# Optimization experiments

Hardware: AMD Instinct MI355X
Metric: run time of the kernel (lower is better)

## Reference

```python
import jax, jax.numpy as jnp
import numpy as np

NUM_GRIDS = 8

def _rbf(x):
    # FastKAN-style radial basis over a fixed grid on [-2, 2]
    grid = jnp.linspace(-2.0, 2.0, NUM_GRIDS).astype(x.dtype)
    h = 4.0 / (NUM_GRIDS - 1)  # grid spacing used as RBF bandwidth
    z = (x[..., None] - grid) / h
    return jnp.exp(-z * z)  # (..., D, G)

def _spline_layer(x, base_w, base_b, spline_w, spline_b):
    # base path: Linear(silu(x)); spline path: Linear(rbf features)
    base = jax.nn.silu(x) @ base_w.T + base_b
    feats = _rbf(x).reshape(x.shape[:-1] + (x.shape[-1] * NUM_GRIDS,))
    return base + feats @ spline_w.T + spline_b


def setup_inputs() -> dict:
    key = jax.random.key(0)
    ks = jax.random.split(key, 12)
    B, Sx, Sy, D = 4, 1024, 1024, 256
    H1, H2 = 128, 64
    def lin(k, o, i):
        return (jax.random.normal(k, (o, i), jnp.float32) / np.sqrt(i)).astype(jnp.float32)
    return {
        "x": jax.random.normal(ks[0], (B, Sx, D), jnp.float32),
        "y": jax.random.normal(ks[1], (B, Sy, D), jnp.float32),
        "base_w1x": lin(ks[2], H1, D), "base_b1x": jnp.zeros((H1,), jnp.float32),
        "spline_w1x": lin(ks[3], H1, D * NUM_GRIDS), "spline_b1x": jnp.zeros((H1,), jnp.float32),
        "base_w2x": lin(ks[4], H2, H1), "base_b2x": jnp.zeros((H2,), jnp.float32),
        "spline_w2x": lin(ks[5], H2, H1 * NUM_GRIDS), "spline_b2x": jnp.zeros((H2,), jnp.float32),
        "base_w1y": lin(ks[6], H1, D), "base_b1y": jnp.zeros((H1,), jnp.float32),
        "spline_w1y": lin(ks[7], H1, D * NUM_GRIDS), "spline_b1y": jnp.zeros((H1,), jnp.float32),
        "base_w2y": lin(ks[8], H2, H1), "base_b2y": jnp.zeros((H2,), jnp.float32),
        "spline_w2y": lin(ks[9], H2, H1 * NUM_GRIDS), "spline_b2y": jnp.zeros((H2,), jnp.float32),
        "final_w": lin(ks[10], 1, 2 * H2), "final_b": jnp.zeros((1,), jnp.float32),
    }


def reference(x, y,
              base_w1x, base_b1x, spline_w1x, spline_b1x,
              base_w2x, base_b2x, spline_w2x, spline_b2x,
              base_w1y, base_b1y, spline_w1y, spline_b1y,
              base_w2y, base_b2y, spline_w2y, spline_b2y,
              final_w, final_b):
    # Per-branch spline stacks: (B, S, D) -> (B, S, H2)
    hx = _spline_layer(_spline_layer(x, base_w1x, base_b1x, spline_w1x, spline_b1x),
                       base_w2x, base_b2x, spline_w2x, spline_b2x)
    hy = _spline_layer(_spline_layer(y, base_w1y, base_b1y, spline_w1y, spline_b1y),
                       base_w2y, base_b2y, spline_w2y, spline_b2y)
    # The original expands to (B, Sx, Sy, 2*H2), applies the affine final
    # layer, then means over all Sx*Sy pairs. By linearity this equals two
    # independent seq-means projected by the split weight, avoiding the
    # quadratic intermediate while computing identical math.
    H2 = hx.shape[-1]
    wx, wy = final_w[:, :H2], final_w[:, H2:]
    out = hx.mean(axis=1) @ wx.T + hy.mean(axis=1) @ wy.T + final_b  # (B, 1)
    return out
```

## Files before the change

kernel.cpp:

```cpp
#include <hip/hip_runtime.h>

typedef __attribute__((ext_vector_type(8))) short short8;
typedef __attribute__((ext_vector_type(16))) float floatx16;


__device__ __forceinline__ unsigned short f2bf(float f) {
  union { float f; unsigned u; } v; v.f = f;
  unsigned r = v.u + 0x7fffu + ((v.u >> 16) & 1u);
  return (unsigned short)(r >> 16);
}

__global__ __launch_bounds__(512) void prep_frags(
    const float* __restrict__ bw1x, const float* __restrict__ sw1x,
    const float* __restrict__ bb1x, const float* __restrict__ sb1x,
    const float* __restrict__ bw2x, const float* __restrict__ sw2x,
    const float* __restrict__ bb2x, const float* __restrict__ sb2x,
    const float* __restrict__ bw1y, const float* __restrict__ sw1y,
    const float* __restrict__ bb1y, const float* __restrict__ sb1y,
    const float* __restrict__ bw2y, const float* __restrict__ sw2y,
    const float* __restrict__ bb2y, const float* __restrict__ sb2y,
    uint4* __restrict__ B1fx, uint4* __restrict__ B1fy,
    uint4* __restrict__ B2fx, uint4* __restrict__ B2fy,
    float* __restrict__ b1x, float* __restrict__ b1y,
    float* __restrict__ b2x, float* __restrict__ b2y,
    int* __restrict__ cnt)
{
  int idx = blockIdx.x * 512 + threadIdx.x;
  if (idx < 2 * 36864) {
    int sid = idx / 36864;
    int rem = idx - sid * 36864;
    int q = rem >> 6, l = rem & 63;
    int nc = q & 3, t9 = q >> 2;
    int j = t9 % 9, ds = t9 / 9;
    const float* bw = sid ? bw1y : bw1x;
    const float* sw = sid ? sw1y : sw1x;
    uint4* dst = sid ? B1fy : B1fx;
    int o = nc * 32 + (l & 31);
    int dbase = ds * 16 + (l >> 5) * 8;
    unsigned short eh[8];
    #pragma unroll
    for (int i = 0; i < 8; ++i) {
      int d = dbase + i;
      float wv = (j == 0) ? bw[o * 256 + d] : sw[o * 2048 + d * 8 + (j - 1)];
      eh[i] = f2bf(wv);
    }
    uint4 oh;
    oh.x = (unsigned)eh[0] | ((unsigned)eh[1] << 16);
    oh.y = (unsigned)eh[2] | ((unsigned)eh[3] << 16);
    oh.z = (unsigned)eh[4] | ((unsigned)eh[5] << 16);
    oh.w = (unsigned)eh[6] | ((unsigned)eh[7] << 16);
    dst[q * 64 + l] = oh;
  } else if (idx < 2 * 36864 + 2 * 9216) {
    int i2 = idx - 2 * 36864;
    int sid = i2 / 9216;
    int rem = i2 - sid * 9216;
    int q2 = rem >> 6, l = rem & 63;
    int nc = q2 & 1, t9 = q2 >> 1;
    int j = t9 % 9, w = t9 / 9;
    const float* bw = sid ? bw2y : bw2x;
    const float* sw = sid ? sw2y : sw2x;
    uint4* dst = sid ? B2fy : B2fx;
    int o = nc * 32 + (l & 31);
    int dbase = w * 16 + (l >> 5) * 8;
    unsigned short eh[8];
    #pragma unroll
    for (int i = 0; i < 8; ++i) {
      int d = dbase + i;
      float wv = (j == 0) ? bw[o * 128 + d] : sw[o * 1024 + d * 8 + (j - 1)];
      eh[i] = f2bf(wv);
    }
    uint4 oh;
    oh.x = (unsigned)eh[0] | ((unsigned)eh[1] << 16);
    oh.y = (unsigned)eh[2] | ((unsigned)eh[3] << 16);
    oh.z = (unsigned)eh[4] | ((unsigned)eh[5] << 16);
    oh.w = (unsigned)eh[6] | ((unsigned)eh[7] << 16);
    dst[q2 * 64 + l] = oh;
  } else {
    int i2 = idx - (2 * 36864 + 2 * 9216);
    if (i2 < 128)      b1x[i2]       = bb1x[i2]       + sb1x[i2];
    else if (i2 < 256) b1y[i2 - 128] = bb1y[i2 - 128] + sb1y[i2 - 128];
    else if (i2 < 320) b2x[i2 - 256] = bb2x[i2 - 256] + sb2x[i2 - 256];
    else if (i2 < 384) b2y[i2 - 320] = bb2y[i2 - 320] + sb2y[i2 - 320];
    else if (i2 < 388) cnt[i2 - 384] = 0;
  }
}

__global__ __launch_bounds__(512, 2) void fused_kernel(
    const float* __restrict__ Xx, const float* __restrict__ Xy,
    const uint4* __restrict__ B1fx, const uint4* __restrict__ B1fy,
    const uint4* __restrict__ B2fx, const uint4* __restrict__ B2fy,
    const float* __restrict__ b1x_, const float* __restrict__ b1y_,
    const float* __restrict__ b2x_, const float* __restrict__ b2y_,
    const float* __restrict__ finw, const float* __restrict__ finb,
    float* __restrict__ partial, int* __restrict__ cnt,
    float* __restrict__ out)
{
  __shared__ __align__(16) char smem[51232];
  float* xsh  = (float*)smem;
  float* S0   = (float*)smem;
  float* S1   = (float*)(smem + 16384);
  float* h1s  = (float*)(smem + 33792);
  float* redw = (float*)(smem + 51200);

  const int t    = threadIdx.x;
  const int bid  = blockIdx.x;
  const int sid  = bid >> 7;
  const int m    = bid & 127;
  const int wave = t >> 6;
  const int l    = t & 63;
  const int lc   = l & 31;
  const int lk   = l >> 5;

  const float* X  = sid ? Xy : Xx;
  const uint4* B1 = sid ? B1fy : B1fx;
  const uint4* B2 = sid ? B2fy : B2fx;
  const float* b1 = sid ? b1y_ : b1x_;
  const float* b2 = sid ? b2y_ : b2x_;

  {
    int row = t >> 4, col = (t & 15) * 16;
    const float* src = X + (size_t)(m * 32 + row) * 256 + col;
    #pragma unroll
    for (int q = 0; q < 4; ++q)
      *(float4*)(xsh + row * 264 + col + q * 4) = *(const float4*)(src + q * 4);
  }
  __syncthreads();

  float xr0[8], xr1[8];
  {
    int cb = wave * 32 + lk * 8;
    float4 v0 = *(const float4*)(xsh + lc * 264 + cb);
    float4 v1 = *(const float4*)(xsh + lc * 264 + cb + 4);
    float4 u0 = *(const float4*)(xsh + lc * 264 + cb + 16);
    float4 u1 = *(const float4*)(xsh + lc * 264 + cb + 20);
    xr0[0]=v0.x; xr0[1]=v0.y; xr0[2]=v0.z; xr0[3]=v0.w;
    xr0[4]=v1.x; xr0[5]=v1.y; xr0[6]=v1.z; xr0[7]=v1.w;
    xr1[0]=u0.x; xr1[1]=u0.y; xr1[2]=u0.z; xr1[3]=u0.w;
    xr1[4]=u1.x; xr1[5]=u1.y; xr1[6]=u1.z; xr1[7]=u1.w;
  }
  __syncthreads();

  floatx16 acc[4] = {};

  auto loadB1 = [&](int s, uint4* bf) {
    int j = s >> 1, ds = wave * 2 + (s & 1);
    const uint4* bp = B1 + (size_t)((ds * 9 + j) * 4) * 64 + l;
    #pragma unroll
    for (int nc = 0; nc < 4; ++nc) bf[nc] = bp[nc * 64];
  };
  auto computeB1 = [&](int s, const uint4* bf) {
    int j = s >> 1;
    const float* xr = (s & 1) ? xr1 : xr0;
    float f[8];
    if (j == 0) {
      #pragma unroll
      for (int i = 0; i < 8; ++i)
        f[i] = __fdividef(xr[i], 1.f + __expf(-xr[i]));
    } else {
      float g = -2.f + (float)(j - 1) * (4.f / 7.f);
      #pragma unroll
      for (int i = 0; i < 8; ++i) {
        float z = (xr[i] - g) * 1.75f;
        f[i] = __expf(-z * z);
      }
    }
    short8 a;
    #pragma unroll
    for (int i = 0; i < 8; ++i) a[i] = (short)f2bf(f[i]);
    #pragma unroll
    for (int nc = 0; nc < 4; ++nc) {
      short8 bh = __builtin_bit_cast(short8, bf[nc]);
      acc[nc] = __builtin_amdgcn_mfma_f32_32x32x16_bf16(a, bh, acc[nc], 0, 0, 0);
    }
  };

  {
    uint4 bfE[4], bfO[4];
    loadB1(0, bfE);
    #pragma unroll 1
    for (int s = 0; s < 18; s += 2) {
      loadB1(s + 1, bfO);
      computeB1(s, bfE);
      if (s + 2 < 18) loadB1(s + 2, bfE);
      computeB1(s + 1, bfO);
    }
  }

  auto st = [&](float* Sb) {
    #pragma unroll
    for (int nc = 0; nc < 4; ++nc)
      #pragma unroll
      for (int r = 0; r < 16; ++r) {
        int row = (r & 3) + 8 * (r >> 2) + 4 * lk;
        Sb[row * 128 + nc * 32 + lc] = acc[nc][r];
      }
  };
  auto ad = [&](const float* Sb) {
    #pragma unroll
    for (int nc = 0; nc < 4; ++nc)
      #pragma unroll
      for (int r = 0; r < 16; ++r) {
        int row = (r & 3) + 8 * (r >> 2) + 4 * lk;
        acc[nc][r] += Sb[row * 128 + nc * 32 + lc];
      }
  };
  __syncthreads();
  if (wave == 1) st(S0);
  if (wave == 3) st(S1);
  __syncthreads();
  if (wave == 0) ad(S0);
  if (wave == 2) ad(S1);
  __syncthreads();
  if (wave == 5) st(S0);
  if (wave == 7) st(S1);
  __syncthreads();
  if (wave == 4) ad(S0);
  if (wave == 6) ad(S1);
  __syncthreads();
  if (wave == 2) st(S0);
  if (wave == 6) st(S1);
  __syncthreads();
  if (wave == 0) ad(S0);
  if (wave == 4) ad(S1);
  __syncthreads();
  if (wave == 4) st(S0);
  __syncthreads();
  if (wave == 0) {
    ad(S0);
    #pragma unroll
    for (int nc = 0; nc < 4; ++nc)
      #pragma unroll
      for (int r = 0; r < 16; ++r) {
        int row = (r & 3) + 8 * (r >> 2) + 4 * lk;
        int col = nc * 32 + lc;
        h1s[row * 136 + col] = acc[nc][r] + b1[col];
      }
  }
  __syncthreads();

  floatx16 acc2[2] = {};

  auto loadB2 = [&](int s, uint4* cf) {
    const uint4* bp = B2 + (size_t)((wave * 9 + s) * 2) * 64 + l;
    #pragma unroll
    for (int nc = 0; nc < 2; ++nc) cf[nc] = bp[nc * 64];
  };

  uint4 cfE[2], cfO[2];
  loadB2(0, cfE);

  float hr[8];
  {
    int cb = wave * 16 + lk * 8;
    float4 v0 = *(const float4*)(h1s + lc * 136 + cb);
    float4 v1 = *(const float4*)(h1s + lc * 136 + cb + 4);
    hr[0]=v0.x; hr[1]=v0.y; hr[2]=v0.z; hr[3]=v0.w;
    hr[4]=v1.x; hr[5]=v1.y; hr[6]=v1.z; hr[7]=v1.w;
  }

  auto computeB2 = [&](int s, const uint4* cf) {
    float f[8];
    if (s == 0) {
      #pragma unroll
      for (int i = 0; i < 8; ++i)
        f[i] = __fdividef(hr[i], 1.f + __expf(-hr[i]));
    } else {
      float g = -2.f + (float)(s - 1) * (4.f / 7.f);
      #pragma unroll
      for (int i = 0; i < 8; ++i) {
        float z = (hr[i] - g) * 1.75f;
        f[i] = __expf(-z * z);
      }
    }
    short8 a;
    #pragma unroll
    for (int i = 0; i < 8; ++i) a[i] = (short)f2bf(f[i]);
    #pragma unroll
    for (int nc = 0; nc < 2; ++nc) {
      short8 bh = __builtin_bit_cast(short8, cf[nc]);
      acc2[nc] = __builtin_amdgcn_mfma_f32_32x32x16_bf16(a, bh, acc2[nc], 0, 0, 0);
    }
  };

  #pragma unroll 1
  for (int s = 0; s < 8; s += 2) {
    loadB2(s + 1, cfO);
    computeB2(s, cfE);
    loadB2(s + 2, cfE);
    computeB2(s + 1, cfO);
  }
  computeB2(8, cfE);

  const float* wf = finw + sid * 64;
  {
    float w0 = wf[lc], w1v = wf[32 + lc];
    float pz = 0.f;
    #pragma unroll
    for (int r = 0; r < 16; ++r) pz += acc2[0][r] * w0 + acc2[1][r] * w1v;
    #pragma unroll
    for (int off = 32; off > 0; off >>= 1) pz += __shfl_down(pz, off, 64);
    if (l == 0) redw[wave] = pz;
  }
  __syncthreads();

  if (wave == 0) {
    const int b    = m >> 5;
    const int slot = sid * 32 + (m & 31);
    float v = (l < 8) ? redw[l] : 0.f;
    v += 32.f * b2[l] * wf[l];
    #pragma unroll
    for (int off = 32; off > 0; off >>= 1) v += __shfl_down(v, off, 64);
    int old = 0;
    if (l == 0) {
      partial[b * 64 + slot] = v;
      __threadfence();
      old = atomicAdd(&cnt[b], 1);
    }
    int bc = __shfl(old, 0, 64);
    if (bc == 63) {
      float pv = atomicAdd(&partial[b * 64 + l], 0.f);
      #pragma unroll
      for (int off = 32; off > 0; off >>= 1) pv += __shfl_down(pv, off, 64);
      if (l == 0) out[b] = finb[0] + pv * (1.0f / 1024.0f);
    }
  }
}

extern "C" void kernel_launch(void* const* d_in, const int* in_sizes, int n_in,
                              void* d_out, int out_size, void* d_ws, size_t ws_size,
                              hipStream_t stream)
{
  (void)in_sizes; (void)n_in; (void)out_size; (void)ws_size;
  const float* x    = (const float*)d_in[0];
  const float* y    = (const float*)d_in[1];
  const float* bw1x = (const float*)d_in[2];
  const float* bb1x = (const float*)d_in[3];
  const float* sw1x = (const float*)d_in[4];
  const float* sb1x = (const float*)d_in[5];
  const float* bw2x = (const float*)d_in[6];
  const float* bb2x = (const float*)d_in[7];
  const float* sw2x = (const float*)d_in[8];
  const float* sb2x = (const float*)d_in[9];
  const float* bw1y = (const float*)d_in[10];
  const float* bb1y = (const float*)d_in[11];
  const float* sw1y = (const float*)d_in[12];
  const float* sb1y = (const float*)d_in[13];
  const float* bw2y = (const float*)d_in[14];
  const float* bb2y = (const float*)d_in[15];
  const float* sw2y = (const float*)d_in[16];
  const float* sb2y = (const float*)d_in[17];
  const float* finw = (const float*)d_in[18];
  const float* finb = (const float*)d_in[19];

  char* ws = (char*)d_ws;
  uint4* B1fx = (uint4*)(ws);
  uint4* B1fy = (uint4*)(ws + 589824);
  uint4* B2fx = (uint4*)(ws + 1179648);
  uint4* B2fy = (uint4*)(ws + 1327104);
  float* b1x  = (float*)(ws + 1474560);
  float* b1y  = b1x + 128;
  float* b2x  = b1y + 128;
  float* b2y  = b2x + 64;
  float* partial = b2y + 64;
  int*   cnt  = (int*)(partial + 256);

  int prep_total = 2 * 36864 + 2 * 9216 + 388;
  int prep_blocks = (prep_total + 511) / 512;
  hipLaunchKernelGGL(prep_frags, dim3(prep_blocks), dim3(512), 0, stream,
                     bw1x, sw1x, bb1x, sb1x, bw2x, sw2x, bb2x, sb2x,
                     bw1y, sw1y, bb1y, sb1y, bw2y, sw2y, bb2y, sb2y,
                     B1fx, B1fy, B2fx, B2fy, b1x, b1y, b2x, b2y, cnt);

  hipLaunchKernelGGL(fused_kernel, dim3(256), dim3(512), 0, stream,
                     x, y, B1fx, B1fy, B2fx, B2fy, b1x, b1y, b2x, b2y,
                     finw, finb, partial, cnt, (float*)d_out);
}
```

Before: 32.54 us.

## Split layer-1 K dimension across two blocks with global partial-sum handoff

Measured after the change: 103.3 us. +217.6%, slower.

```diff
diff --git a/kernel.cpp b/kernel.cpp
--- a/kernel.cpp
+++ b/kernel.cpp
@@ -23,7 +23,7 @@
     uint4* __restrict__ B2fx, uint4* __restrict__ B2fy,
     float* __restrict__ b1x, float* __restrict__ b1y,
     float* __restrict__ b2x, float* __restrict__ b2y,
-    int* __restrict__ cnt)
+    int* __restrict__ cnts)
 {
   int idx = blockIdx.x * 512 + threadIdx.x;
   if (idx < 2 * 36864) {
@@ -81,35 +81,38 @@
     else if (i2 < 256) b1y[i2 - 128] = bb1y[i2 - 128] + sb1y[i2 - 128];
     else if (i2 < 320) b2x[i2 - 256] = bb2x[i2 - 256] + sb2x[i2 - 256];
     else if (i2 < 384) b2y[i2 - 320] = bb2y[i2 - 320] + sb2y[i2 - 320];
-    else if (i2 < 388) cnt[i2 - 384] = 0;
+    else if (i2 < 384 + 260) cnts[i2 - 384] = 0;
   }
 }
 
-__global__ __launch_bounds__(512, 2) void fused_kernel(
+__global__ __launch_bounds__(256, 4) void fused_kernel(
     const float* __restrict__ Xx, const float* __restrict__ Xy,
     const uint4* __restrict__ B1fx, const uint4* __restrict__ B1fy,
     const uint4* __restrict__ B2fx, const uint4* __restrict__ B2fy,
     const float* __restrict__ b1x_, const float* __restrict__ b1y_,
     const float* __restrict__ b2x_, const float* __restrict__ b2y_,
     const float* __restrict__ finw, const float* __restrict__ finb,
-    float* __restrict__ partial, int* __restrict__ cnt,
+    float* __restrict__ hp, float* __restrict__ partial,
+    int* __restrict__ cnt_tile, int* __restrict__ cnt_batch,
     float* __restrict__ out)
 {
-  __shared__ __align__(16) char smem[51232];
+  __shared__ __align__(16) char smem[33824];
   float* xsh  = (float*)smem;
   float* S0   = (float*)smem;
-  float* S1   = (float*)(smem + 16384);
-  float* h1s  = (float*)(smem + 33792);
-  float* redw = (float*)(smem + 51200);
+  float* S1   = (float*)(smem + 16896);
+  float* redw = (float*)(smem + 33280);
+  int*   flag = (int*)(smem + 33296);
 
   const int t    = threadIdx.x;
   const int bid  = blockIdx.x;
-  const int sid  = bid >> 7;
-  const int m    = bid & 127;
+  const int sid  = bid >> 8;
+  const int m    = (bid >> 1) & 127;
+  const int kh   = bid & 1;
   const int wave = t >> 6;
   const int l    = t & 63;
   const int lc   = l & 31;
   const int lk   = l >> 5;
+  const int tile = sid * 128 + m;
 
   const float* X  = sid ? Xy : Xx;
   const uint4* B1 = sid ? B1fy : B1fx;
@@ -118,21 +121,21 @@
   const float* b2 = sid ? b2y_ : b2x_;
 
   {
-    int row = t >> 4, col = (t & 15) * 16;
-    const float* src = X + (size_t)(m * 32 + row) * 256 + col;
+    int row = t >> 3, col = (t & 7) * 16;
+    const float* src = X + (size_t)(m * 32 + row) * 256 + kh * 128 + col;
     #pragma unroll
     for (int q = 0; q < 4; ++q)
-      *(float4*)(xsh + row * 264 + col + q * 4) = *(const float4*)(src + q * 4);
+      *(float4*)(xsh + row * 132 + col + q * 4) = *(const float4*)(src + q * 4);
   }
   __syncthreads();
 
   float xr0[8], xr1[8];
   {
     int cb = wave * 32 + lk * 8;
-    float4 v0 = *(const float4*)(xsh + lc * 264 + cb);
-    float4 v1 = *(const float4*)(xsh + lc * 264 + cb + 4);
-    float4 u0 = *(const float4*)(xsh + lc * 264 + cb + 16);
-    float4 u1 = *(const float4*)(xsh + lc * 264 + cb + 20);
+    float4 v0 = *(const float4*)(xsh + lc * 132 + cb);
+    float4 v1 = *(const float4*)(xsh + lc * 132 + cb + 4);
+    float4 u0 = *(const float4*)(xsh + lc * 132 + cb + 16);
+    float4 u1 = *(const float4*)(xsh + lc * 132 + cb + 20);
     xr0[0]=v0.x; xr0[1]=v0.y; xr0[2]=v0.z; xr0[3]=v0.w;
     xr0[4]=v1.x; xr0[5]=v1.y; xr0[6]=v1.z; xr0[7]=v1.w;
     xr1[0]=u0.x; xr1[1]=u0.y; xr1[2]=u0.z; xr1[3]=u0.w;
@@ -143,7 +146,7 @@
   floatx16 acc[4] = {};
 
   auto loadB1 = [&](int s, uint4* bf) {
-    int j = s >> 1, ds = wave * 2 + (s & 1);
+    int j = s >> 1, ds = kh * 8 + wave * 2 + (s & 1);
     const uint4* bp = B1 + (size_t)((ds * 9 + j) * 4) * 64 + l;
     #pragma unroll
     for (int nc = 0; nc < 4; ++nc) bf[nc] = bp[nc * 64];
@@ -211,61 +214,57 @@
   if (wave == 0) ad(S0);
   if (wave == 2) ad(S1);
   __syncthreads();
-  if (wave == 5) st(S0);
-  if (wave == 7) st(S1);
-  __syncthreads();
-  if (wave == 4) ad(S0);
-  if (wave == 6) ad(S1);
-  __syncthreads();
   if (wave == 2) st(S0);
-  if (wave == 6) st(S1);
-  __syncthreads();
-  if (wave == 0) ad(S0);
-  if (wave == 4) ad(S1);
-  __syncthreads();
-  if (wave == 4) st(S0);
   __syncthreads();
   if (wave == 0) {
     ad(S0);
+    float* dst = hp + (size_t)(tile * 2 + kh) * 4096;
     #pragma unroll
     for (int nc = 0; nc < 4; ++nc)
       #pragma unroll
       for (int r = 0; r < 16; ++r) {
         int row = (r & 3) + 8 * (r >> 2) + 4 * lk;
-        int col = nc * 32 + lc;
-        h1s[row * 136 + col] = acc[nc][r] + b1[col];
-      }
-  }
-  __syncthreads();
+        dst[row * 128 + nc * 32 + lc] = acc[nc][r];
+      }
+    __threadfence();
+    if (l == 0) flag[0] = atomicAdd(&cnt_tile[tile], 1);
+  }
+  __syncthreads();
+  if (flag[0] == 0) return;
+
+  const float* hpA = hp + (size_t)(tile * 2 + 0) * 4096;
+  const float* hpB = hp + (size_t)(tile * 2 + 1) * 4096;
+  float hr0[8], hr1[8];
+  {
+    int col0 = wave * 32 + lk * 8;
+    #pragma unroll
+    for (int i = 0; i < 8; ++i) {
+      hr0[i] = atomicAdd((float*)&hpA[lc * 128 + col0 + i], 0.f)
+             + atomicAdd((float*)&hpB[lc * 128 + col0 + i], 0.f)
+             + b1[col0 + i];
+      hr1[i] = atomicAdd((float*)&hpA[lc * 128 + col0 + 16 + i], 0.f)
+             + atomicAdd((float*)&hpB[lc * 128 + col0 + 16 + i], 0.f)
+             + b1[col0 + 16 + i];
+    }
+  }
 
   floatx16 acc2[2] = {};
-
   auto loadB2 = [&](int s, uint4* cf) {
-    const uint4* bp = B2 + (size_t)((wave * 9 + s) * 2) * 64 + l;
+    int j = s >> 1, w = wave * 2 + (s & 1);
+    const uint4* bp = B2 + (size_t)((w * 9 + j) * 2) * 64 + l;
     #pragma unroll
     for (int nc = 0; nc < 2; ++nc) cf[nc] = bp[nc * 64];
   };
-
-  uint4 cfE[2], cfO[2];
-  loadB2(0, cfE);
-
-  float hr[8];
-  {
-    int cb = wave * 16 + lk * 8;
-    float4 v0 = *(const float4*)(h1s + lc * 136 + cb);
-    float4 v1 = *(const float4*)(h1s + lc * 136 + cb + 4);
-    hr[0]=v0.x; hr[1]=v0.y; hr[2]=v0.z; hr[3]=v0.w;
-    hr[4]=v1.x; hr[5]=v1.y; hr[6]=v1.z; hr[7]=v1.w;
-  }
-
   auto computeB2 = [&](int s, const uint4* cf) {
+    int j = s >> 1;
+    const float* hr = (s & 1) ? hr1 : hr0;
     float f[8];
-    if (s == 0) {
+    if (j == 0) {
       #pragma unroll
       for (int i = 0; i < 8; ++i)
         f[i] = __fdividef(hr[i], 1.f + __expf(-hr[i]));
     } else {
-      float g = -2.f + (float)(s - 1) * (4.f / 7.f);
+      float g = -2.f + (float)(j - 1) * (4.f / 7.f);
       #pragma unroll
       for (int i = 0; i < 8; ++i) {
         float z = (hr[i] - g) * 1.75f;
@@ -282,14 +281,17 @@
     }
   };
 
-  #pragma unroll 1
-  for (int s = 0; s < 8; s += 2) {
-    loadB2(s + 1, cfO);
-    computeB2(s, cfE);
-    loadB2(s + 2, cfE);
-    computeB2(s + 1, cfO);
-  }
-  computeB2(8, cfE);
+  {
+    uint4 cfE[2], cfO[2];
+    loadB2(0, cfE);
+    #pragma unroll 1
+    for (int s = 0; s < 18; s += 2) {
+      loadB2(s + 1, cfO);
+      computeB2(s, cfE);
+      if (s + 2 < 18) loadB2(s + 2, cfE);
+      computeB2(s + 1, cfO);
+    }
+  }
 
   const float* wf = finw + sid * 64;
   {
@@ -306,7 +308,7 @@
   if (wave == 0) {
     const int b    = m >> 5;
     const int slot = sid * 32 + (m & 31);
-    float v = (l < 8) ? redw[l] : 0.f;
+    float v = (l < 4) ? redw[l] : 0.f;
     v += 32.f * b2[l] * wf[l];
     #pragma unroll
     for (int off = 32; off > 0; off >>= 1) v += __shfl_down(v, off, 64);
@@ -314,7 +316,7 @@
     if (l == 0) {
       partial[b * 64 + slot] = v;
       __threadfence();
-      old = atomicAdd(&cnt[b], 1);
+      old = atomicAdd(&cnt_batch[b], 1);
     }
     int bc = __shfl(old, 0, 64);
     if (bc == 63) {
@@ -362,16 +364,20 @@
   float* b2x  = b1y + 128;
   float* b2y  = b2x + 64;
   float* partial = b2y + 64;
-  int*   cnt  = (int*)(partial + 256);
-
-  int prep_total = 2 * 36864 + 2 * 9216 + 388;
+  int*   cnts = (int*)(partial + 256);
+  int*   cnt_tile  = cnts;
+  int*   cnt_batch = cnts + 256;
+  float* hp   = (float*)(ws + 1572864);
+
+  int prep_total = 2 * 36864 + 2 * 9216 + 384 + 260;
   int prep_blocks = (prep_total + 511) / 512;
   hipLaunchKernelGGL(prep_frags, dim3(prep_blocks), dim3(512), 0, stream,
                      bw1x, sw1x, bb1x, sb1x, bw2x, sw2x, bb2x, sb2x,
                      bw1y, sw1y, bb1y, sb1y, bw2y, sw2y, bb2y, sb2y,
-                     B1fx, B1fy, B2fx, B2fy, b1x, b1y, b2x, b2y, cnt);
-
-  hipLaunchKernelGGL(fused_kernel, dim3(256), dim3(512), 0, stream,
+                     B1fx, B1fy, B2fx, B2fy, b1x, b1y, b2x, b2y, cnts);
+
+  hipLaunchKernelGGL(fused_kernel, dim3(512), dim3(256), 0, stream,
                      x, y, B1fx, B1fy, B2fx, B2fy, b1x, b1y, b2x, b2y,
-                     finw, finb, partial, cnt, (float*)d_out);
+                     finw, finb, hp, partial, cnt_tile, cnt_batch,
+                     (float*)d_out);
 }
```

## Retile fused KAN kernel to 64-row tiles with split hidden columns

Applied to the files above, without the earlier changes.

New measurement: 36.38 us. +11.8%, slower.

```diff
diff --git a/kernel.cpp b/kernel.cpp
--- a/kernel.cpp
+++ b/kernel.cpp
@@ -23,7 +23,7 @@
     uint4* __restrict__ B2fx, uint4* __restrict__ B2fy,
     float* __restrict__ b1x, float* __restrict__ b1y,
     float* __restrict__ b2x, float* __restrict__ b2y,
-    int* __restrict__ cnt)
+    int* __restrict__ cnts)
 {
   int idx = blockIdx.x * 512 + threadIdx.x;
   if (idx < 2 * 36864) {
@@ -50,23 +50,28 @@
     oh.z = (unsigned)eh[4] | ((unsigned)eh[5] << 16);
     oh.w = (unsigned)eh[6] | ((unsigned)eh[7] << 16);
     dst[q * 64 + l] = oh;
-  } else if (idx < 2 * 36864 + 2 * 9216) {
+  } else if (idx < 2 * 36864 + 2 * 10240) {
     int i2 = idx - 2 * 36864;
-    int sid = i2 / 9216;
-    int rem = i2 - sid * 9216;
-    int q2 = rem >> 6, l = rem & 63;
-    int nc = q2 & 1, t9 = q2 >> 1;
-    int j = t9 % 9, w = t9 / 9;
+    int sid = i2 / 10240;
+    int rem = i2 - sid * 10240;
+    int q2n = rem >> 6, l = rem & 63;
+    int nc2 = q2n & 1, t5 = q2n >> 1;
+    int s = t5 % 5, wn = t5 / 5;
+    int nh = wn >> 3, w = wn & 7;
     const float* bw = sid ? bw2y : bw2x;
     const float* sw = sid ? sw2y : sw2x;
     uint4* dst = sid ? B2fy : B2fx;
-    int o = nc * 32 + (l & 31);
-    int dbase = w * 16 + (l >> 5) * 8;
+    int o = nc2 * 32 + (l & 31);
+    int p = s * 2 + (l >> 5);
+    int dbase = nh * 64 + w * 8;
     unsigned short eh[8];
     #pragma unroll
     for (int i = 0; i < 8; ++i) {
       int d = dbase + i;
-      float wv = (j == 0) ? bw[o * 128 + d] : sw[o * 1024 + d * 8 + (j - 1)];
+      float wv;
+      if (p == 0)       wv = bw[o * 128 + d];
+      else if (p < 9)   wv = sw[o * 1024 + d * 8 + (p - 1)];
+      else              wv = 0.f;
       eh[i] = f2bf(wv);
     }
     uint4 oh;
@@ -74,14 +79,14 @@
     oh.y = (unsigned)eh[2] | ((unsigned)eh[3] << 16);
     oh.z = (unsigned)eh[4] | ((unsigned)eh[5] << 16);
     oh.w = (unsigned)eh[6] | ((unsigned)eh[7] << 16);
-    dst[q2 * 64 + l] = oh;
+    dst[q2n * 64 + l] = oh;
   } else {
-    int i2 = idx - (2 * 36864 + 2 * 9216);
+    int i2 = idx - (2 * 36864 + 2 * 10240);
     if (i2 < 128)      b1x[i2]       = bb1x[i2]       + sb1x[i2];
     else if (i2 < 256) b1y[i2 - 128] = bb1y[i2 - 128] + sb1y[i2 - 128];
     else if (i2 < 320) b2x[i2 - 256] = bb2x[i2 - 256] + sb2x[i2 - 256];
     else if (i2 < 384) b2y[i2 - 320] = bb2y[i2 - 320] + sb2y[i2 - 320];
-    else if (i2 < 388) cnt[i2 - 384] = 0;
+    else if (i2 < 388) cnts[i2 - 384] = 0;
   }
 }
 
@@ -92,20 +97,21 @@
     const float* __restrict__ b1x_, const float* __restrict__ b1y_,
     const float* __restrict__ b2x_, const float* __restrict__ b2y_,
     const float* __restrict__ finw, const float* __restrict__ finb,
-    float* __restrict__ partial, int* __restrict__ cnt,
+    float* __restrict__ partial, int* __restrict__ cnt_batch,
     float* __restrict__ out)
 {
-  __shared__ __align__(16) char smem[51232];
-  float* xsh  = (float*)smem;
+  __shared__ __align__(16) char smem[50240];
   float* S0   = (float*)smem;
   float* S1   = (float*)(smem + 16384);
-  float* h1s  = (float*)(smem + 33792);
-  float* redw = (float*)(smem + 51200);
+  float* h1s  = (float*)(smem + 32768);
+  float* redw = (float*)(smem + 50176);
 
   const int t    = threadIdx.x;
   const int bid  = blockIdx.x;
   const int sid  = bid >> 7;
-  const int m    = bid & 127;
+  const int rem  = bid & 127;
+  const int mt   = rem >> 1;
+  const int nh   = rem & 1;
   const int wave = t >> 6;
   const int l    = t & 63;
   const int lc   = l & 31;
@@ -117,65 +123,65 @@
   const float* b1 = sid ? b1y_ : b1x_;
   const float* b2 = sid ? b2y_ : b2x_;
 
+  float xr[2][2][8];
   {
-    int row = t >> 4, col = (t & 15) * 16;
-    const float* src = X + (size_t)(m * 32 + row) * 256 + col;
-    #pragma unroll
-    for (int q = 0; q < 4; ++q)
-      *(float4*)(xsh + row * 264 + col + q * 4) = *(const float4*)(src + q * 4);
-  }
-  __syncthreads();
-
-  float xr0[8], xr1[8];
-  {
-    int cb = wave * 32 + lk * 8;
-    float4 v0 = *(const float4*)(xsh + lc * 264 + cb);
-    float4 v1 = *(const float4*)(xsh + lc * 264 + cb + 4);
-    float4 u0 = *(const float4*)(xsh + lc * 264 + cb + 16);
-    float4 u1 = *(const float4*)(xsh + lc * 264 + cb + 20);
-    xr0[0]=v0.x; xr0[1]=v0.y; xr0[2]=v0.z; xr0[3]=v0.w;
-    xr0[4]=v1.x; xr0[5]=v1.y; xr0[6]=v1.z; xr0[7]=v1.w;
-    xr1[0]=u0.x; xr1[1]=u0.y; xr1[2]=u0.z; xr1[3]=u0.w;
-    xr1[4]=u1.x; xr1[5]=u1.y; xr1[6]=u1.z; xr1[7]=u1.w;
-  }
-  __syncthreads();
-
-  floatx16 acc[4] = {};
+    const float* xb = X + (size_t)(mt * 64) * 256 + wave * 32 + lk * 8;
+    #pragma unroll
+    for (int rg = 0; rg < 2; ++rg) {
+      const float* rp = xb + (size_t)(lc + rg * 32) * 256;
+      float4 a0 = *(const float4*)(rp);
+      float4 a1 = *(const float4*)(rp + 4);
+      float4 c0 = *(const float4*)(rp + 16);
+      float4 c1 = *(const float4*)(rp + 20);
+      xr[rg][0][0]=a0.x; xr[rg][0][1]=a0.y; xr[rg][0][2]=a0.z; xr[rg][0][3]=a0.w;
+      xr[rg][0][4]=a1.x; xr[rg][0][5]=a1.y; xr[rg][0][6]=a1.z; xr[rg][0][7]=a1.w;
+      xr[rg][1][0]=c0.x; xr[rg][1][1]=c0.y; xr[rg][1][2]=c0.z; xr[rg][1][3]=c0.w;
+      xr[rg][1][4]=c1.x; xr[rg][1][5]=c1.y; xr[rg][1][6]=c1.z; xr[rg][1][7]=c1.w;
+    }
+  }
+
+  floatx16 acc[2][2] = {};
 
   auto loadB1 = [&](int s, uint4* bf) {
     int j = s >> 1, ds = wave * 2 + (s & 1);
-    const uint4* bp = B1 + (size_t)((ds * 9 + j) * 4) * 64 + l;
-    #pragma unroll
-    for (int nc = 0; nc < 4; ++nc) bf[nc] = bp[nc * 64];
+    const uint4* bp = B1 + (size_t)((ds * 9 + j) * 4 + nh * 2) * 64 + l;
+    bf[0] = bp[0];
+    bf[1] = bp[64];
   };
   auto computeB1 = [&](int s, const uint4* bf) {
-    int j = s >> 1;
-    const float* xr = (s & 1) ? xr1 : xr0;
-    float f[8];
-    if (j == 0) {
-      #pragma unroll
-      for (int i = 0; i < 8; ++i)
-        f[i] = __fdividef(xr[i], 1.f + __expf(-xr[i]));
-    } else {
-      float g = -2.f + (float)(j - 1) * (4.f / 7.f);
-      #pragma unroll
-      for (int i = 0; i < 8; ++i) {
-        float z = (xr[i] - g) * 1.75f;
-        f[i] = __expf(-z * z);
+    int j = s >> 1, dh = s & 1;
+    short8 a[2];
+    #pragma unroll
+    for (int rg = 0; rg < 2; ++rg) {
+      float f[8];
+      if (j == 0) {
+        #pragma unroll
+        for (int i = 0; i < 8; ++i) {
+          float xv = xr[rg][dh][i];
+          f[i] = __fdividef(xv, 1.f + __expf(-xv));
+        }
+      } else {
+        float g = -2.f + (float)(j - 1) * (4.f / 7.f);
+        #pragma unroll
+        for (int i = 0; i < 8; ++i) {
+          float z = (xr[rg][dh][i] - g) * 1.75f;
+          f[i] = __expf(-z * z);
+        }
       }
-    }
-    short8 a;
-    #pragma unroll
-    for (int i = 0; i < 8; ++i) a[i] = (short)f2bf(f[i]);
-    #pragma unroll
-    for (int nc = 0; nc < 4; ++nc) {
-      short8 bh = __builtin_bit_cast(short8, bf[nc]);
-      acc[nc] = __builtin_amdgcn_mfma_f32_32x32x16_bf16(a, bh, acc[nc], 0, 0, 0);
-    }
+      #pragma unroll
+      for (int i = 0; i < 8; ++i) a[rg][i] = (short)f2bf(f[i]);
+    }
+    #pragma unroll
+    for (int rg = 0; rg < 2; ++rg)
+      #pragma unroll
+      for (int nc = 0; nc < 2; ++nc) {
+        short8 bh = __builtin_bit_cast(short8, bf[nc]);
+        acc[rg][nc] = __builtin_amdgcn_mfma_f32_32x32x16_bf16(a[rg], bh, acc[rg][nc], 0, 0, 0);
+      }
   };
 
   {
-    uint4 bfE[4], bfO[4];
+    uint4 bfE[2], bfO[2];
     loadB1(0, bfE);
     #pragma unroll 1
     for (int s = 0; s < 18; s += 2) {
@@ -188,21 +194,25 @@
 
   auto st = [&](float* Sb) {
     #pragma unroll
-    for (int nc = 0; nc < 4; ++nc)
-      #pragma unroll
-      for (int r = 0; r < 16; ++r) {
-        int row = (r & 3) + 8 * (r >> 2) + 4 * lk;
-        Sb[row * 128 + nc * 32 + lc] = acc[nc][r];
-      }
+    for (int rg = 0; rg < 2; ++rg)
+      #pragma unroll
+      for (int nc = 0; nc < 2; ++nc)
+        #pragma unroll
+        for (int r = 0; r < 16; ++r) {
+          int row = rg * 32 + (r & 3) + 8 * (r >> 2) + 4 * lk;
+          Sb[row * 64 + nc * 32 + lc] = acc[rg][nc][r];
+        }
   };
   auto ad = [&](const float* Sb) {
     #pragma unroll
-    for (int nc = 0; nc < 4; ++nc)
-      #pragma unroll
-      for (int r = 0; r < 16; ++r) {
-        int row = (r & 3) + 8 * (r >> 2) + 4 * lk;
-        acc[nc][r] += Sb[row * 128 + nc * 32 + lc];
-      }
+    for (int rg = 0; rg < 2; ++rg)
+      #pragma unroll
+      for (int nc = 0; nc < 2; ++nc)
+        #pragma unroll
+        for (int r = 0; r < 16; ++r) {
+          int row = rg * 32 + (r & 3) + 8 * (r >> 2) + 4 * lk;
+          acc[rg][nc][r] += Sb[row * 64 + nc * 32 + lc];
+        }
   };
   __syncthreads();
   if (wave == 1) st(S0);
@@ -228,75 +238,88 @@
   if (wave == 0) {
     ad(S0);
     #pragma unroll
-    for (int nc = 0; nc < 4; ++nc)
-      #pragma unroll
-      for (int r = 0; r < 16; ++r) {
-        int row = (r & 3) + 8 * (r >> 2) + 4 * lk;
-        int col = nc * 32 + lc;
-        h1s[row * 136 + col] = acc[nc][r] + b1[col];
+    for (int rg = 0; rg < 2; ++rg)
+      #pragma unroll
+      for (int nc = 0; nc < 2; ++nc)
+        #pragma unroll
+        for (int r = 0; r < 16; ++r) {
+          int row = rg * 32 + (r & 3) + 8 * (r >> 2) + 4 * lk;
+          int colL = nc * 32 + lc;
+          h1s[row * 68 + colL] = acc[rg][nc][r] + b1[nh * 64 + colL];
+        }
+  }
+  __syncthreads();
+
+  float hr[2][8];
+  {
+    #pragma unroll
+    for (int rg = 0; rg < 2; ++rg) {
+      const float* rp = h1s + (size_t)(lc + rg * 32) * 68 + wave * 8;
+      float4 v0 = *(const float4*)(rp);
+      float4 v1 = *(const float4*)(rp + 4);
+      hr[rg][0]=v0.x; hr[rg][1]=v0.y; hr[rg][2]=v0.z; hr[rg][3]=v0.w;
+      hr[rg][4]=v1.x; hr[rg][5]=v1.y; hr[rg][6]=v1.z; hr[rg][7]=v1.w;
+    }
+  }
+
+  floatx16 acc2[2][2] = {};
+  auto loadB2 = [&](int s, uint4* cf) {
+    const uint4* bp = B2 + (size_t)((((nh * 8 + wave) * 5 + s) * 2)) * 64 + l;
+    cf[0] = bp[0];
+    cf[1] = bp[64];
+  };
+  auto computeB2 = [&](int s, const uint4* cf) {
+    int p = s * 2 + lk;
+    short8 a[2];
+    #pragma unroll
+    for (int rg = 0; rg < 2; ++rg) {
+      float f[8];
+      if (p == 0) {
+        #pragma unroll
+        for (int i = 0; i < 8; ++i) {
+          float hv = hr[rg][i];
+          f[i] = __fdividef(hv, 1.f + __expf(-hv));
+        }
+      } else if (p == 9) {
+        #pragma unroll
+        for (int i = 0; i < 8; ++i) f[i] = 0.f;
+      } else {
+        float g = -2.f + (float)(p - 1) * (4.f / 7.f);
+        #pragma unroll
+        for (int i = 0; i < 8; ++i) {
+          float z = (hr[rg][i] - g) * 1.75f;
+          f[i] = __expf(-z * z);
+        }
       }
-  }
-  __syncthreads();
-
-  floatx16 acc2[2] = {};
-
-  auto loadB2 = [&](int s, uint4* cf) {
-    const uint4* bp = B2 + (size_t)((wave * 9 + s) * 2) * 64 + l;
-    #pragma unroll
-    for (int nc = 0; nc < 2; ++nc) cf[nc] = bp[nc * 64];
-  };
-
-  uint4 cfE[2], cfO[2];
-  loadB2(0, cfE);
-
-  float hr[8];
+      #pragma unroll
+      for (int i = 0; i < 8; ++i) a[rg][i] = (short)f2bf(f[i]);
+    }
+    #pragma unroll
+    for (int rg = 0; rg < 2; ++rg)
+      #pragma unroll
+      for (int nc2 = 0; nc2 < 2; ++nc2) {
+        short8 bh = __builtin_bit_cast(short8, cf[nc2]);
+        acc2[rg][nc2] = __builtin_amdgcn_mfma_f32_32x32x16_bf16(a[rg], bh, acc2[rg][nc2], 0, 0, 0);
+      }
+  };
+
   {
-    int cb = wave * 16 + lk * 8;
-    float4 v0 = *(const float4*)(h1s + lc * 136 + cb);
-    float4 v1 = *(const float4*)(h1s + lc * 136 + cb + 4);
-    hr[0]=v0.x; hr[1]=v0.y; hr[2]=v0.z; hr[3]=v0.w;
-    hr[4]=v1.x; hr[5]=v1.y; hr[6]=v1.z; hr[7]=v1.w;
-  }
-
-  auto computeB2 = [&](int s, const uint4* cf) {
-    float f[8];
-    if (s == 0) {
-      #pragma unroll
-      for (int i = 0; i < 8; ++i)
-        f[i] = __fdividef(hr[i], 1.f + __expf(-hr[i]));
-    } else {
-      float g = -2.f + (float)(s - 1) * (4.f / 7.f);
-      #pragma unroll
-      for (int i = 0; i < 8; ++i) {
-        float z = (hr[i] - g) * 1.75f;
-        f[i] = __expf(-z * z);
-      }
-    }
-    short8 a;
-    #pragma unroll
-    for (int i = 0; i < 8; ++i) a[i] = (short)f2bf(f[i]);
-    #pragma unroll
-    for (int nc = 0; nc < 2; ++nc) {
-      short8 bh = __builtin_bit_cast(short8, cf[nc]);
-      acc2[nc] = __builtin_amdgcn_mfma_f32_32x32x16_bf16(a, bh, acc2[nc], 0, 0, 0);
-    }
-  };
-
-  #pragma unroll 1
-  for (int s = 0; s < 8; s += 2) {
-    loadB2(s + 1, cfO);
-    computeB2(s, cfE);
-    loadB2(s + 2, cfE);
-    computeB2(s + 1, cfO);
-  }
-  computeB2(8, cfE);
+    uint4 cfE[2], cfO[2];
+    loadB2(0, cfE);
+    loadB2(1, cfO); computeB2(0, cfE); loadB2(2, cfE); computeB2(1, cfO);
+    loadB2(3, cfO); computeB2(2, cfE); loadB2(4, cfE); computeB2(3, cfO);
+    computeB2(4, cfE);
+  }
 
   const float* wf = finw + sid * 64;
   {
     float w0 = wf[lc], w1v = wf[32 + lc];
     float pz = 0.f;
     #pragma unroll
-    for (int r = 0; r < 16; ++r) pz += acc2[0][r] * w0 + acc2[1][r] * w1v;
+    for (int rg = 0; rg < 2; ++rg)
+      #pragma unroll
+      for (int r = 0; r < 16; ++r)
+        pz += acc2[rg][0][r] * w0 + acc2[rg][1][r] * w1v;
     #pragma unroll
     for (int off = 32; off > 0; off >>= 1) pz += __shfl_down(pz, off, 64);
     if (l == 0) redw[wave] = pz;
@@ -304,17 +327,17 @@
   __syncthreads();
 
   if (wave == 0) {
-    const int b    = m >> 5;
-    const int slot = sid * 32 + (m & 31);
+    const int b    = rem >> 5;
+    const int slot = sid * 32 + (rem & 31);
     float v = (l < 8) ? redw[l] : 0.f;
-    v += 32.f * b2[l] * wf[l];
+    if (nh == 0) v += 64.f * b2[l] * wf[l];
     #pragma unroll
     for (int off = 32; off > 0; off >>= 1) v += __shfl_down(v, off, 64);
     int old = 0;
     if (l == 0) {
       partial[b * 64 + slot] = v;
       __threadfence();
-      old = atomicAdd(&cnt[b], 1);
+      old = atomicAdd(&cnt_batch[b], 1);
     }
     int bc = __shfl(old, 0, 64);
     if (bc == 63) {
@@ -356,22 +379,22 @@
   uint4* B1fx = (uint4*)(ws);
   uint4* B1fy = (uint4*)(ws + 589824);
   uint4* B2fx = (uint4*)(ws + 1179648);
-  uint4* B2fy = (uint4*)(ws + 1327104);
-  float* b1x  = (float*)(ws + 1474560);
+  uint4* B2fy = (uint4*)(ws + 1343488);
+  float* b1x  = (float*)(ws + 1507328);
   float* b1y  = b1x + 128;
   float* b2x  = b1y + 128;
   float* b2y  = b2x + 64;
   float* partial = b2y + 64;
-  int*   cnt  = (int*)(partial + 256);
-
-  int prep_total = 2 * 36864 + 2 * 9216 + 388;
+  int*   cnt_batch = (int*)(partial + 256);
+
+  int prep_total = 2 * 36864 + 2 * 10240 + 388;
   int prep_blocks = (prep_total + 511) / 512;
   hipLaunchKernelGGL(prep_frags, dim3(prep_blocks), dim3(512), 0, stream,
                      bw1x, sw1x, bb1x, sb1x, bw2x, sw2x, bb2x, sb2x,
                      bw1y, sw1y, bb1y, sb1y, bw2y, sw2y, bb2y, sb2y,
-                     B1fx, B1fy, B2fx, B2fy, b1x, b1y, b2x, b2y, cnt);
+                     B1fx, B1fy, B2fx, B2fy, b1x, b1y, b2x, b2y, cnt_batch);
 
   hipLaunchKernelGGL(fused_kernel, dim3(256), dim3(512), 0, stream,
                      x, y, B1fx, B1fy, B2fx, B2fy, b1x, b1y, b2x, b2y,
-                     finw, finb, partial, cnt, (float*)d_out);
+                     finw, finb, partial, cnt_batch, (float*)d_out);
 }
```
